# Optimization experiments

Hardware: AMD Instinct MI355X
Metric: run time of the kernel (lower is better)

## Reference

```python
import jax, jax.numpy as jnp
import numpy as np

N = 100000      # nodes
E = 3200000     # edges (avg degree 32)
DIN, DH, DOUT = 128, 32, 2


def setup_inputs() -> dict:
    key = jax.random.key(0)
    k1, k2, k3, k4 = jax.random.split(key, 4)
    x = jax.random.normal(k1, (N, DIN), dtype=jnp.float32)
    edge_index = jax.random.randint(k2, (2, E), 0, N, dtype=jnp.int64)
    # Glorot-ish scaled weights
    W1 = jax.random.normal(k3, (DIN, DH), dtype=jnp.float32) / np.sqrt(DIN)
    b1 = jnp.zeros((DH,), dtype=jnp.float32)
    W2 = jax.random.normal(k4, (DH, DOUT), dtype=jnp.float32) / np.sqrt(DH)
    b2 = jnp.zeros((DOUT,), dtype=jnp.float32)
    return {"x": x, "edge_index": edge_index, "W1": W1, "b1": b1, "W2": W2, "b2": b2}


def reference(x, edge_index, W1, b1, W2, b2):
    n = x.shape[0]
    # GCNConv default: add self-loops, symmetric deg^{-1/2} A deg^{-1/2} normalization
    loops = jnp.arange(n, dtype=edge_index.dtype)
    src = jnp.concatenate([edge_index[0], loops])  # [E+N]
    dst = jnp.concatenate([edge_index[1], loops])  # [E+N]
    deg = jax.ops.segment_sum(jnp.ones_like(dst, dtype=x.dtype), dst, num_segments=n)
    dinv = jnp.where(deg > 0, jax.lax.rsqrt(deg), 0.0)
    norm = dinv[src] * dinv[dst]  # [E+N]

    def gcn_layer(h, W, b):
        m = h @ W                                   # [n, dout] transform first (PyG order)
        msgs = m[src] * norm[:, None]               # gather + scale  [E+N, dout]
        agg = jax.ops.segment_sum(msgs, dst, num_segments=n)  # scatter-add
        return agg + b

    h = jax.nn.relu(gcn_layer(x, W1, b1))
    return gcn_layer(h, W2, b2)
```

## Files before the change

kernel.cpp:

```cpp
#include <hip/hip_runtime.h>
#include <hip/hip_bf16.h>

#define DIN 128
#define DH 32
#define DOUT 2
#define NPB 128
#define NPB_SHIFT 7
#define NBUK_MAX 1024
#define FILL_EDGES 8192
#define ECHUNK 2048
#define CAP 5632

#define FXS1 2048.0f
#define FXI1 (1.0f / 2048.0f)
#define FXS2 131072.0f
#define FXI2 (1.0f / 131072.0f)


__device__ inline int sxlo(unsigned int w) { return (int)(short)(w & 0xFFFFu); }
__device__ inline int sxhi(unsigned int w) { return ((int)w) >> 16; }

__global__ void zero_kernel(int* __restrict__ gcur, int nbuk,
                            unsigned int* __restrict__ mqrow) {
    int i = blockIdx.x * blockDim.x + threadIdx.x;
    if (i < nbuk) gcur[i] = 0;
    if (blockIdx.x == 0 && threadIdx.x < 16) mqrow[threadIdx.x] = 0u;
}

__global__ void __launch_bounds__(1024, 2)
binfill_kernel(const int* __restrict__ src, const int* __restrict__ dst,
               int* __restrict__ gcur, unsigned int* __restrict__ binned,
               int e, int nbuk) {
    __shared__ int cnt[NBUK_MAX];
    __shared__ int pos[NBUK_MAX];
    __shared__ int gb[NBUK_MAX];
    __shared__ int stmp[1024];
    __shared__ unsigned int sorted[FILL_EDGES];
    __shared__ unsigned short aux[FILL_EDGES];

    int t = threadIdx.x;
    int e0 = blockIdx.x * FILL_EDGES;
    int m = min(FILL_EDGES, e - e0);

    if (t < nbuk) cnt[t] = 0;
    __syncthreads();
    for (int i = t; i < m; i += 1024) atomicAdd(&cnt[dst[e0 + i] >> NPB_SHIFT], 1);
    __syncthreads();

    int v = (t < nbuk) ? cnt[t] : 0;
    stmp[t] = v;
    __syncthreads();
    for (int off = 1; off < 1024; off <<= 1) {
        int x = (t >= off) ? stmp[t - off] : 0;
        __syncthreads();
        stmp[t] += x;
        __syncthreads();
    }
    if (t < nbuk) pos[t] = stmp[t] - v;
    __syncthreads();

    for (int i = t; i < m; i += 1024) {
        int d = dst[e0 + i];
        int sv = src[e0 + i];
        int b = d >> NPB_SHIFT;
        int r = atomicAdd(&pos[b], 1);
        sorted[r] = ((unsigned int)(d & (NPB - 1)) << 17) | (unsigned int)sv;
        aux[r] = (unsigned short)b;
    }
    __syncthreads();

    if (t < nbuk) {
        int c = cnt[t];
        gb[t] = c ? atomicAdd(&gcur[t], c) : 0;
    }
    __syncthreads();

    for (int i = t; i < m; i += 1024) {
        int b = aux[i];
        int start = pos[b] - cnt[b];
        unsigned int off = (unsigned int)(gb[b] + (i - start));
        if (off < (unsigned int)CAP)
            binned[(size_t)b * CAP + off] = sorted[i];
    }
}

__global__ void bdinv_kernel(const int* __restrict__ gcur,
                             const unsigned int* __restrict__ binned,
                             float* __restrict__ dinv, int n) {
    __shared__ int cnt[NPB];
    int t = threadIdx.x;
    int b = blockIdx.x;
    if (t < NPB) cnt[t] = 0;
    __syncthreads();
    const unsigned int* bp = binned + (size_t)b * CAP;
    const int cntb = min(gcur[b], CAP);
    for (int i = t; i < cntb; i += 256) atomicAdd(&cnt[bp[i] >> 17], 1);
    __syncthreads();
    if (t < NPB) {
        int r = (b << NPB_SHIFT) + t;
        if (r < n) dinv[r] = rsqrtf((float)(cnt[t] + 1));
    }
}

#define XTS 68
__global__ void __launch_bounds__(128, 4)
gemm1_kernel(const float* __restrict__ x, const float* __restrict__ W1,
             const float* __restrict__ dinv,
             short* __restrict__ mqc, int n) {
    __shared__ float  XT[DIN * XTS];
    __shared__ float4 Wl4[DIN * 8];

    int t = threadIdx.x;
    for (int i = t; i < DIN * 8; i += 128) Wl4[i] = ((const float4*)W1)[i];

    int rb = blockIdx.x * 64;
    for (int i = t; i < 64 * 32; i += 128) {
        int r = i & 63, kq = i >> 6;
        int gr = rb + r;
        float4 v = make_float4(0.f, 0.f, 0.f, 0.f);
        if (gr < n) v = ((const float4*)x)[(size_t)gr * 32 + kq];
        XT[(4 * kq + 0) * XTS + r] = v.x;
        XT[(4 * kq + 1) * XTS + r] = v.y;
        XT[(4 * kq + 2) * XTS + r] = v.z;
        XT[(4 * kq + 3) * XTS + r] = v.w;
    }
    __syncthreads();

    const int cq = t & 7;
    const int rq = t >> 3;
    float4 a0 = make_float4(0.f, 0.f, 0.f, 0.f);
    float4 a1 = a0, a2 = a0, a3 = a0;
#pragma unroll 8
    for (int k = 0; k < DIN; ++k) {
        float4 xv = *(const float4*)&XT[k * XTS + 4 * rq];
        float4 w  = Wl4[k * 8 + cq];
        a0.x += xv.x * w.x; a0.y += xv.x * w.y; a0.z += xv.x * w.z; a0.w += xv.x * w.w;
        a1.x += xv.y * w.x; a1.y += xv.y * w.y; a1.z += xv.y * w.z; a1.w += xv.y * w.w;
        a2.x += xv.z * w.x; a2.y += xv.z * w.y; a2.z += xv.z * w.z; a2.w += xv.z * w.w;
        a3.x += xv.w * w.x; a3.y += xv.w * w.y; a3.z += xv.w * w.z; a3.w += xv.w * w.w;
    }
#pragma unroll
    for (int m = 0; m < 4; ++m) {
        int r = rb + 4 * rq + m;
        if (r < n) {
            float di = dinv[r] * FXS1;
            float4 av = (m == 0) ? a0 : (m == 1) ? a1 : (m == 2) ? a2 : a3;
            short4 sv;
            sv.x = (short)__float2int_rn(av.x * di);
            sv.y = (short)__float2int_rn(av.y * di);
            sv.z = (short)__float2int_rn(av.z * di);
            sv.w = (short)__float2int_rn(av.w * di);
            *(short4*)&mqc[(size_t)r * DH + 4 * cq] = sv;
        }
    }
}

__global__ void __launch_bounds__(512, 8)
agg1_kernel(const int* __restrict__ gcur,
            const unsigned int* __restrict__ binned,
            const short* __restrict__ mqc,
            const float* __restrict__ dinv,
            const float* __restrict__ b1, const float* __restrict__ W2,
            int2* __restrict__ m2qi, int n) {
    __shared__ int acc[NPB * 33];
    __shared__ unsigned int ebuf[2][ECHUNK];

    const int t = threadIdx.x;
    const int b = blockIdx.x;
    const int cntb = min(gcur[b], CAP);
    const int r0 = b << NPB_SHIFT;

    for (int i = t; i < NPB * 33; i += 512) acc[i] = 0;

    const unsigned int* __restrict__ bp = binned + (size_t)b * CAP;
    const unsigned int* __restrict__ mq32 = (const unsigned int*)mqc;
    const unsigned int sent = (unsigned int)n;
    const int nchunks = (cntb + ECHUNK - 1) / ECHUNK;

    unsigned int st[4];
    if (nchunks > 0) {
#pragma unroll
        for (int k = 0; k < 4; ++k) {
            int idx = t + k * 512;
            st[k] = (idx < cntb) ? __builtin_nontemporal_load(&bp[idx]) : sent;
        }
#pragma unroll
        for (int k = 0; k < 4; ++k) ebuf[0][t + k * 512] = st[k];
    }
    __syncthreads();

    const int g = t >> 4, l = t & 15;

    for (int c = 0; c < nchunks; ++c) {
        if (c + 1 < nchunks) {
            const int base = (c + 1) * ECHUNK;
#pragma unroll
            for (int k = 0; k < 4; ++k) {
                int idx = base + t + k * 512;
                st[k] = (idx < cntb) ? __builtin_nontemporal_load(&bp[idx]) : sent;
            }
        }
        const unsigned int* eb = ebuf[c & 1];
        for (int j = 0; j < 64; j += 8) {
            const unsigned int* ej = &eb[g + 32 * j];
            unsigned int e0 = ej[0],   e1 = ej[32],  e2 = ej[64],  e3 = ej[96];
            unsigned int e4 = ej[128], e5 = ej[160], e6 = ej[192], e7 = ej[224];
            unsigned int w0 = mq32[(e0 & 0x1FFFFu) * 16u + l];
            unsigned int w1 = mq32[(e1 & 0x1FFFFu) * 16u + l];
            unsigned int w2 = mq32[(e2 & 0x1FFFFu) * 16u + l];
            unsigned int w3 = mq32[(e3 & 0x1FFFFu) * 16u + l];
            unsigned int w4 = mq32[(e4 & 0x1FFFFu) * 16u + l];
            unsigned int w5 = mq32[(e5 & 0x1FFFFu) * 16u + l];
            unsigned int w6 = mq32[(e6 & 0x1FFFFu) * 16u + l];
            unsigned int w7 = mq32[(e7 & 0x1FFFFu) * 16u + l];
            int d0 = (int)(e0 >> 17) * 33 + 2 * l;
            int d1 = (int)(e1 >> 17) * 33 + 2 * l;
            int d2 = (int)(e2 >> 17) * 33 + 2 * l;
            int d3 = (int)(e3 >> 17) * 33 + 2 * l;
            int d4 = (int)(e4 >> 17) * 33 + 2 * l;
            int d5 = (int)(e5 >> 17) * 33 + 2 * l;
            int d6 = (int)(e6 >> 17) * 33 + 2 * l;
            int d7 = (int)(e7 >> 17) * 33 + 2 * l;
            atomicAdd(&acc[d0], sxlo(w0)); atomicAdd(&acc[d0 + 1], sxhi(w0));
            atomicAdd(&acc[d1], sxlo(w1)); atomicAdd(&acc[d1 + 1], sxhi(w1));
            atomicAdd(&acc[d2], sxlo(w2)); atomicAdd(&acc[d2 + 1], sxhi(w2));
            atomicAdd(&acc[d3], sxlo(w3)); atomicAdd(&acc[d3 + 1], sxhi(w3));
            atomicAdd(&acc[d4], sxlo(w4)); atomicAdd(&acc[d4 + 1], sxhi(w4));
            atomicAdd(&acc[d5], sxlo(w5)); atomicAdd(&acc[d5 + 1], sxhi(w5));
            atomicAdd(&acc[d6], sxlo(w6)); atomicAdd(&acc[d6 + 1], sxhi(w6));
            atomicAdd(&acc[d7], sxlo(w7)); atomicAdd(&acc[d7 + 1], sxhi(w7));
        }
        __syncthreads();
        if (c + 1 < nchunks) {
#pragma unroll
            for (int k = 0; k < 4; ++k) ebuf[(c + 1) & 1][t + k * 512] = st[k];
        }
        __syncthreads();
    }

    const int j = t >> 2, q = t & 3;
    const int r = r0 + j;
    if (r < n) {
        const float di = dinv[r];
        const unsigned int* srow = (const unsigned int*)mqc + (size_t)r * 16 + q * 4;
        const int* ar = &acc[j * 33 + q * 8];
        float p0 = 0.f, p1 = 0.f;
#pragma unroll
        for (int k = 0; k < 4; ++k) {
            unsigned int sw = srow[k];
            int c = q * 8 + 2 * k;
            float h0 = fmaxf(di * (float)(ar[2 * k]     + sxlo(sw)) * FXI1 + b1[c],     0.0f);
            float h1 = fmaxf(di * (float)(ar[2 * k + 1] + sxhi(sw)) * FXI1 + b1[c + 1], 0.0f);
            p0 += h0 * W2[2 * c]     + h1 * W2[2 * c + 2];
            p1 += h0 * W2[2 * c + 1] + h1 * W2[2 * c + 3];
        }
        p0 += __shfl_down(p0, 2, 4); p0 += __shfl_down(p0, 1, 4);
        p1 += __shfl_down(p1, 2, 4); p1 += __shfl_down(p1, 1, 4);
        if (q == 0)
            m2qi[r] = make_int2(__float2int_rn(di * p0 * FXS2),
                                __float2int_rn(di * p1 * FXS2));
    }
}

__global__ void __launch_bounds__(256, 4)
agg2_kernel(const int* __restrict__ gcur,
            const unsigned int* __restrict__ binned,
            const int2* __restrict__ m2qi,
            const float* __restrict__ dinv, const float* __restrict__ b2,
            float* __restrict__ out, int n) {
    __shared__ int a0s[NPB], a1s[NPB];
    const int t = threadIdx.x;
    const int b = blockIdx.x;
    const int cntb = min(gcur[b], CAP);
    const int r0 = b << NPB_SHIFT;

    if (t < NPB) { a0s[t] = 0; a1s[t] = 0; }
    __syncthreads();

    const unsigned int* __restrict__ bp = binned + (size_t)b * CAP;
    int i = t;
    for (; i + 768 < cntb; i += 1024) {
        unsigned int e0 = __builtin_nontemporal_load(&bp[i]);
        unsigned int e1 = __builtin_nontemporal_load(&bp[i + 256]);
        unsigned int e2 = __builtin_nontemporal_load(&bp[i + 512]);
        unsigned int e3 = __builtin_nontemporal_load(&bp[i + 768]);
        int2 v0 = m2qi[e0 & 0x1FFFFu];
        int2 v1 = m2qi[e1 & 0x1FFFFu];
        int2 v2 = m2qi[e2 & 0x1FFFFu];
        int2 v3 = m2qi[e3 & 0x1FFFFu];
        atomicAdd(&a0s[e0 >> 17], v0.x); atomicAdd(&a1s[e0 >> 17], v0.y);
        atomicAdd(&a0s[e1 >> 17], v1.x); atomicAdd(&a1s[e1 >> 17], v1.y);
        atomicAdd(&a0s[e2 >> 17], v2.x); atomicAdd(&a1s[e2 >> 17], v2.y);
        atomicAdd(&a0s[e3 >> 17], v3.x); atomicAdd(&a1s[e3 >> 17], v3.y);
    }
    for (; i < cntb; i += 256) {
        unsigned int e0 = __builtin_nontemporal_load(&bp[i]);
        int2 v0 = m2qi[e0 & 0x1FFFFu];
        atomicAdd(&a0s[e0 >> 17], v0.x); atomicAdd(&a1s[e0 >> 17], v0.y);
    }
    __syncthreads();

    if (t < NPB) {
        int r = r0 + t;
        if (r < n) {
            float di = dinv[r];
            int2 self = m2qi[r];
            out[(size_t)r * DOUT + 0] = di * (float)(a0s[t] + self.x) * FXI2 + b2[0];
            out[(size_t)r * DOUT + 1] = di * (float)(a1s[t] + self.y) * FXI2 + b2[1];
        }
    }
}

extern "C" void kernel_launch(void* const* d_in, const int* in_sizes, int n_in,
                              void* d_out, int out_size, void* d_ws, size_t ws_size,
                              hipStream_t stream) {
    const float* x  = (const float*)d_in[0];
    const int*   ei = (const int*)d_in[1];
    const float* W1 = (const float*)d_in[2];
    const float* b1 = (const float*)d_in[3];
    const float* W2 = (const float*)d_in[4];
    const float* b2 = (const float*)d_in[5];
    float* out = (float*)d_out;

    const int n = in_sizes[0] / DIN;
    const int e = in_sizes[1] / 2;
    const int* src = ei;
    const int* dst = ei + e;
    const int nbuk = (n + NPB - 1) >> NPB_SHIFT;

    char* ws = (char*)d_ws;
    float* dinv   = (float*)ws;          ws += (size_t)n * 4;
    int* gcur     = (int*)ws;            ws += NBUK_MAX * 4;
    unsigned int* binned = (unsigned int*)ws;   ws += (size_t)nbuk * CAP * 4;
    short* mqc    = (short*)ws;          ws += ((size_t)n + 1) * DH * 2;
    int2* m2qi    = (int2*)ws;

    const int B = 256;
    const int fill_blocks = (e + FILL_EDGES - 1) / FILL_EDGES;

    zero_kernel<<<(nbuk + B - 1) / B, B, 0, stream>>>(
        gcur, nbuk, (unsigned int*)(mqc + (size_t)n * DH));
    binfill_kernel<<<fill_blocks, 1024, 0, stream>>>(src, dst, gcur, binned, e, nbuk);
    bdinv_kernel<<<nbuk, B, 0, stream>>>(gcur, binned, dinv, n);
    gemm1_kernel<<<(n + 63) / 64, 128, 0, stream>>>(x, W1, dinv, mqc, n);
    agg1_kernel<<<nbuk, 512, 0, stream>>>(gcur, binned, mqc, dinv, b1, W2, m2qi, n);
    agg2_kernel<<<nbuk, B, 0, stream>>>(gcur, binned, m2qi, dinv, b2, out, n);
}
```

Baseline: 221.4 us.

## Fold degree counting into binfill and drop the separate dinv kernel

Drops the bdinv kernel, which re-read every binned edge to count in-degree. Degrees are now accumulated with global atomics on a per-node array inside binfill, and gemm1 computes rsqrt of the degree itself and writes dinv for the later stages. The change trades one full pass over the binned edges and a launch for about 3.2M scattered global atomics in binfill. It also zeroes the new degree array in zero_kernel and doubles agg2's block size to 512 threads.

```diff
diff --git a/kernel.cpp b/kernel.cpp
--- a/kernel.cpp
+++ b/kernel.cpp
@@ -21,16 +21,18 @@
 __device__ inline int sxhi(unsigned int w) { return ((int)w) >> 16; }
 
 __global__ void zero_kernel(int* __restrict__ gcur, int nbuk,
+                            int* __restrict__ degarr, int n,
                             unsigned int* __restrict__ mqrow) {
-    int i = blockIdx.x * blockDim.x + threadIdx.x;
+    int i = blockIdx.x * 256 + threadIdx.x;
     if (i < nbuk) gcur[i] = 0;
-    if (blockIdx.x == 0 && threadIdx.x < 16) mqrow[threadIdx.x] = 0u;
+    if (i < 16) mqrow[i] = 0u;
+    for (int k = i; k < n; k += gridDim.x * 256) degarr[k] = 0;
 }
 
 __global__ void __launch_bounds__(1024, 2)
 binfill_kernel(const int* __restrict__ src, const int* __restrict__ dst,
                int* __restrict__ gcur, unsigned int* __restrict__ binned,
-               int e, int nbuk) {
+               int* __restrict__ degarr, int e, int nbuk) {
     __shared__ int cnt[NBUK_MAX];
     __shared__ int pos[NBUK_MAX];
     __shared__ int gb[NBUK_MAX];
@@ -63,6 +65,7 @@
         int d = dst[e0 + i];
         int sv = src[e0 + i];
         int b = d >> NPB_SHIFT;
+        atomicAdd(&degarr[d], 1);
         int r = atomicAdd(&pos[b], 1);
         sorted[r] = ((unsigned int)(d & (NPB - 1)) << 17) | (unsigned int)sv;
         aux[r] = (unsigned short)b;
@@ -84,28 +87,10 @@
     }
 }
 
-__global__ void bdinv_kernel(const int* __restrict__ gcur,
-                             const unsigned int* __restrict__ binned,
-                             float* __restrict__ dinv, int n) {
-    __shared__ int cnt[NPB];
-    int t = threadIdx.x;
-    int b = blockIdx.x;
-    if (t < NPB) cnt[t] = 0;
-    __syncthreads();
-    const unsigned int* bp = binned + (size_t)b * CAP;
-    const int cntb = min(gcur[b], CAP);
-    for (int i = t; i < cntb; i += 256) atomicAdd(&cnt[bp[i] >> 17], 1);
-    __syncthreads();
-    if (t < NPB) {
-        int r = (b << NPB_SHIFT) + t;
-        if (r < n) dinv[r] = rsqrtf((float)(cnt[t] + 1));
-    }
-}
-
 #define XTS 68
 __global__ void __launch_bounds__(128, 4)
 gemm1_kernel(const float* __restrict__ x, const float* __restrict__ W1,
-             const float* __restrict__ dinv,
+             const int* __restrict__ degarr, float* __restrict__ dinv,
              short* __restrict__ mqc, int n) {
     __shared__ float  XT[DIN * XTS];
     __shared__ float4 Wl4[DIN * 8];
@@ -143,7 +128,9 @@
     for (int m = 0; m < 4; ++m) {
         int r = rb + 4 * rq + m;
         if (r < n) {
-            float di = dinv[r] * FXS1;
+            float dd = rsqrtf((float)(degarr[r] + 1));
+            if (cq == 0) dinv[r] = dd;
+            float di = dd * FXS1;
             float4 av = (m == 0) ? a0 : (m == 1) ? a1 : (m == 2) ? a2 : a3;
             short4 sv;
             sv.x = (short)__float2int_rn(av.x * di);
@@ -262,7 +249,7 @@
     }
 }
 
-__global__ void __launch_bounds__(256, 4)
+__global__ void __launch_bounds__(512, 4)
 agg2_kernel(const int* __restrict__ gcur,
             const unsigned int* __restrict__ binned,
             const int2* __restrict__ m2qi,
@@ -279,11 +266,11 @@
 
     const unsigned int* __restrict__ bp = binned + (size_t)b * CAP;
     int i = t;
-    for (; i + 768 < cntb; i += 1024) {
+    for (; i + 1536 < cntb; i += 2048) {
         unsigned int e0 = __builtin_nontemporal_load(&bp[i]);
-        unsigned int e1 = __builtin_nontemporal_load(&bp[i + 256]);
-        unsigned int e2 = __builtin_nontemporal_load(&bp[i + 512]);
-        unsigned int e3 = __builtin_nontemporal_load(&bp[i + 768]);
+        unsigned int e1 = __builtin_nontemporal_load(&bp[i + 512]);
+        unsigned int e2 = __builtin_nontemporal_load(&bp[i + 1024]);
+        unsigned int e3 = __builtin_nontemporal_load(&bp[i + 1536]);
         int2 v0 = m2qi[e0 & 0x1FFFFu];
         int2 v1 = m2qi[e1 & 0x1FFFFu];
         int2 v2 = m2qi[e2 & 0x1FFFFu];
@@ -293,7 +280,7 @@
         atomicAdd(&a0s[e2 >> 17], v2.x); atomicAdd(&a1s[e2 >> 17], v2.y);
         atomicAdd(&a0s[e3 >> 17], v3.x); atomicAdd(&a1s[e3 >> 17], v3.y);
     }
-    for (; i < cntb; i += 256) {
+    for (; i < cntb; i += 512) {
         unsigned int e0 = __builtin_nontemporal_load(&bp[i]);
         int2 v0 = m2qi[e0 & 0x1FFFFu];
         atomicAdd(&a0s[e0 >> 17], v0.x); atomicAdd(&a1s[e0 >> 17], v0.y);
@@ -331,6 +318,7 @@
     char* ws = (char*)d_ws;
     float* dinv   = (float*)ws;          ws += (size_t)n * 4;
     int* gcur     = (int*)ws;            ws += NBUK_MAX * 4;
+    int* degarr   = (int*)ws;            ws += (size_t)n * 4;
     unsigned int* binned = (unsigned int*)ws;   ws += (size_t)nbuk * CAP * 4;
     short* mqc    = (short*)ws;          ws += ((size_t)n + 1) * DH * 2;
     int2* m2qi    = (int2*)ws;
@@ -338,11 +326,11 @@
     const int B = 256;
     const int fill_blocks = (e + FILL_EDGES - 1) / FILL_EDGES;
 
-    zero_kernel<<<(nbuk + B - 1) / B, B, 0, stream>>>(
-        gcur, nbuk, (unsigned int*)(mqc + (size_t)n * DH));
-    binfill_kernel<<<fill_blocks, 1024, 0, stream>>>(src, dst, gcur, binned, e, nbuk);
-    bdinv_kernel<<<nbuk, B, 0, stream>>>(gcur, binned, dinv, n);
-    gemm1_kernel<<<(n + 63) / 64, 128, 0, stream>>>(x, W1, dinv, mqc, n);
+    zero_kernel<<<(n + B - 1) / B, B, 0, stream>>>(
+        gcur, nbuk, degarr, n, (unsigned int*)(mqc + (size_t)n * DH));
+    binfill_kernel<<<fill_blocks, 1024, 0, stream>>>(src, dst, gcur, binned,
+                                                     degarr, e, nbuk);
+    gemm1_kernel<<<(n + 63) / 64, 128, 0, stream>>>(x, W1, degarr, dinv, mqc, n);
     agg1_kernel<<<nbuk, 512, 0, stream>>>(gcur, binned, mqc, dinv, b1, W2, m2qi, n);
-    agg2_kernel<<<nbuk, B, 0, stream>>>(gcur, binned, m2qi, dinv, b2, out, n);
-}
+    agg2_kernel<<<nbuk, 512, 0, stream>>>(gcur, binned, m2qi, dinv, b2, out, n);
+}
```

New measurement: 329.9 us. 49.0% more time.
